# Performance work log

Hardware: AMD Instinct MI355X
Metric: run time of the kernel (lower is better)

The kernel has to match this reference:

```python
import jax, jax.numpy as jnp
import numpy as np

MUL = 32          # channel multiplicity
N_NODES = 50000
N_EDGES = 800000
IN_DIM = 4 * MUL      # 32x0e + 32x1o (ir_mul layout: 1o block is (3, MUL))
SH_DIM = 4            # 0e + 1o
W_DIM = 5 * MUL       # 5 CG paths, per-channel weights
OUT_DIM = 7 * MUL     # 32x0e + 32x1o + 32x1e
INV_SQRT3 = 0.5773502691896258
INV_SQRT2 = 0.7071067811865476


def setup_inputs() -> dict:
    key = jax.random.key(0)
    k1, k2, k3, k4 = jax.random.split(key, 4)
    node_features = jax.random.normal(k1, (N_NODES, IN_DIM), dtype=jnp.float32)
    edge_angular = jax.random.normal(k2, (N_EDGES, SH_DIM), dtype=jnp.float32)
    edge_index = jax.random.randint(k3, (N_EDGES, 2), 0, N_NODES, dtype=jnp.int64)
    tp_weights = jax.random.normal(k4, (N_EDGES, W_DIM), dtype=jnp.float32)
    return {"node_features": node_features, "edge_angular": edge_angular,
            "edge_index": edge_index, "tp_weights": tp_weights}


def reference(node_features, edge_angular, edge_index, tp_weights):
    n_nodes = node_features.shape[0]
    src = edge_index[:, 0]
    dst = edge_index[:, 1]

    # gather sender node features per edge
    h = node_features[src]                       # (E, 4*MUL)
    h0 = h[:, :MUL]                              # (E, MUL)       32x0e
    h1 = h[:, MUL:].reshape(-1, 3, MUL)          # (E, 3, MUL)    32x1o, ir_mul layout

    y0 = edge_angular[:, 0:1]                    # (E, 1)   0e
    y1 = edge_angular[:, 1:4]                    # (E, 3)   1o

    w = tp_weights.reshape(-1, 5, MUL)           # (E, 5, MUL) per-path per-channel

    # path 0: 0e (x) 0e -> 0e ; path 3: 1o (x) 1o -> 0e (dot / sqrt(3))
    dot = jnp.einsum('emc,em->ec', h1, y1)       # (E, MUL)
    out0e = w[:, 0] * h0 * y0 + w[:, 3] * (INV_SQRT3 * dot)

    # path 1: 0e (x) 1o -> 1o ; path 2: 1o (x) 0e -> 1o
    out1o = (w[:, 1][:, None, :] * h0[:, None, :] * y1[:, :, None]
             + w[:, 2][:, None, :] * h1 * y0[:, :, None])     # (E, 3, MUL)

    # path 4: 1o (x) 1o -> 1e (cross / sqrt(2))
    c0 = h1[:, 1] * y1[:, 2, None] - h1[:, 2] * y1[:, 1, None]
    c1 = h1[:, 2] * y1[:, 0, None] - h1[:, 0] * y1[:, 2, None]
    c2 = h1[:, 0] * y1[:, 1, None] - h1[:, 1] * y1[:, 0, None]
    cross = jnp.stack([c0, c1, c2], axis=1)                   # (E, 3, MUL)
    out1e = w[:, 4][:, None, :] * (INV_SQRT2 * cross)

    msg = jnp.concatenate([out0e,
                           out1o.reshape(-1, 3 * MUL),
                           out1e.reshape(-1, 3 * MUL)], axis=1)  # (E, 7*MUL)

    # scatter-add messages into receiver nodes (size_out = n_nodes)
    out = jax.ops.segment_sum(msg, dst, num_segments=n_nodes)    # (N, 7*MUL)
    return out
```

## Files before the change

kernel.cpp:

```cpp
#include <hip/hip_runtime.h>


#define IN_DIM 128
#define W_DIM 160
#define OUT_DIM 224

__device__ __forceinline__ float elem(const float4& v, int i) {
    return ((const float*)&v)[i];
}

__global__ void __launch_bounds__(256) hist_dst(
    const int* __restrict__ eidx, int* __restrict__ counts, int n_edges)
{
    int e = blockIdx.x * blockDim.x + threadIdx.x;
    if (e >= n_edges) return;
    atomicAdd(counts + eidx[2 * e + 1], 1);
}

__global__ void __launch_bounds__(1024) scan_counts(
    int* __restrict__ counts,
    int* __restrict__ cursor,
    int n)
{
    __shared__ int buf[1024];
    __shared__ int carry_s;
    int tid = threadIdx.x;
    if (tid == 0) carry_s = 0;
    __syncthreads();

    for (int base = 0; base < n; base += 1024) {
        int idx = base + tid;
        int x = (idx < n) ? counts[idx] : 0;
        buf[tid] = x;
        __syncthreads();
        #pragma unroll
        for (int off = 1; off < 1024; off <<= 1) {
            int v = (tid >= off) ? buf[tid - off] : 0;
            __syncthreads();
            buf[tid] += v;
            __syncthreads();
        }
        int carry = carry_s;
        int excl = buf[tid] - x + carry;
        if (idx < n) {
            counts[idx] = excl;
            cursor[idx] = excl;
        }
        int chunk_total = buf[1023];
        __syncthreads();
        if (tid == 0) carry_s = carry + chunk_total;
        __syncthreads();
    }
    if (tid == 0) counts[n] = carry_s;
}

__global__ void __launch_bounds__(256) scatter_edges(
    const int* __restrict__ eidx, int* __restrict__ cursor,
    int2* __restrict__ pairs, int n_edges)
{
    int e = blockIdx.x * blockDim.x + threadIdx.x;
    if (e >= n_edges) return;
    int src = eidx[2 * e];
    int dst = eidx[2 * e + 1];
    int pos = atomicAdd(cursor + dst, 1);
    pairs[pos] = make_int2(e, src);
}

__global__ void __launch_bounds__(256) gather_nodes(
    const float* __restrict__ nf,
    const float* __restrict__ ang,
    const float* __restrict__ w,
    const int*  __restrict__ offsets,
    const int2* __restrict__ pairs,
    float* __restrict__ out,
    int n_nodes)
{
    const float INV_SQRT3 = 0.5773502691896258f;
    const float INV_SQRT2 = 0.7071067811865476f;

    int gtid = blockIdx.x * blockDim.x + threadIdx.x;
    int node = gtid >> 6;
    if (node >= n_nodes) return;
    int lane = threadIdx.x & 63;
    int c    = lane & 31;
    int half = lane >> 5;

    int start = offsets[node];
    int end   = offsets[node + 1];

    float a0 = 0.f, a1 = 0.f, a2 = 0.f, a3 = 0.f, a4 = 0.f, a5 = 0.f, a6 = 0.f;

    for (int i = start + half; i < end; i += 2) {
        int2 p = pairs[i];
        int e = p.x, s = p.y;

        float4 y = *(const float4*)(ang + 4 * (size_t)e);

        const float* hp = nf + (size_t)s * IN_DIM + c;
        float h0 = hp[0];
        float ha = hp[32];
        float hb = hp[64];
        float hc = hp[96];

        const float* wp = w + (size_t)e * W_DIM + c;
        float w0 = wp[0];
        float w1 = wp[32];
        float w2 = wp[64];
        float w3 = wp[96];
        float w4 = wp[128];

        float dot = ha * y.y + hb * y.z + hc * y.w;
        a0 += w0 * h0 * y.x + w3 * (INV_SQRT3 * dot);
        a1 += w1 * h0 * y.y + w2 * ha * y.x;
        a2 += w1 * h0 * y.z + w2 * hb * y.x;
        a3 += w1 * h0 * y.w + w2 * hc * y.x;
        float w4s = w4 * INV_SQRT2;
        a4 += w4s * (hb * y.w - hc * y.z);
        a5 += w4s * (hc * y.y - ha * y.w);
        a6 += w4s * (ha * y.z - hb * y.y);
    }

    a0 += __shfl_xor(a0, 32);
    a1 += __shfl_xor(a1, 32);
    a2 += __shfl_xor(a2, 32);
    a3 += __shfl_xor(a3, 32);
    a4 += __shfl_xor(a4, 32);
    a5 += __shfl_xor(a5, 32);
    a6 += __shfl_xor(a6, 32);

    if (half == 0) {
        float* op = out + (size_t)node * OUT_DIM + c;
        op[0]   = a0;
        op[32]  = a1;
        op[64]  = a2;
        op[96]  = a3;
        op[128] = a4;
        op[160] = a5;
        op[192] = a6;
    }
}

__global__ void __launch_bounds__(256) conv_tp_edges_atomic(
    const float* __restrict__ nf,
    const float* __restrict__ ang,
    const int*   __restrict__ eidx,
    const float* __restrict__ w,
    float* __restrict__ out,
    int n_edges)
{
    const float INV_SQRT3 = 0.5773502691896258f;
    const float INV_SQRT2 = 0.7071067811865476f;

    int tid = blockIdx.x * blockDim.x + threadIdx.x;
    int e = tid >> 3;
    int t = tid & 7;
    if (e >= n_edges) return;

    int src = eidx[2 * e];
    int dst = eidx[2 * e + 1];
    float4 y = *(const float4*)(ang + 4 * (size_t)e);

    const float* hp = nf + (size_t)src * IN_DIM + 4 * t;
    float4 h0  = *(const float4*)(hp);
    float4 h1a = *(const float4*)(hp + 32);
    float4 h1b = *(const float4*)(hp + 64);
    float4 h1c = *(const float4*)(hp + 96);

    const float* wp = w + (size_t)e * W_DIM + 4 * t;
    float4 w0 = *(const float4*)(wp);
    float4 w1 = *(const float4*)(wp + 32);
    float4 w2 = *(const float4*)(wp + 64);
    float4 w3 = *(const float4*)(wp + 96);
    float4 w4 = *(const float4*)(wp + 128);

    float* op = out + (size_t)dst * OUT_DIM + 4 * t;

    #pragma unroll
    for (int i = 0; i < 4; ++i) {
        float h0c = elem(h0, i), ha = elem(h1a, i), hb = elem(h1b, i), hc = elem(h1c, i);
        float dot = ha * y.y + hb * y.z + hc * y.w;
        atomicAdd(op + i, elem(w0, i) * h0c * y.x + elem(w3, i) * (INV_SQRT3 * dot));
        float w1c = elem(w1, i), w2c = elem(w2, i);
        atomicAdd(op + 32 + i, w1c * h0c * y.y + w2c * ha * y.x);
        atomicAdd(op + 64 + i, w1c * h0c * y.z + w2c * hb * y.x);
        atomicAdd(op + 96 + i, w1c * h0c * y.w + w2c * hc * y.x);
        float w4c = elem(w4, i) * INV_SQRT2;
        atomicAdd(op + 128 + i, w4c * (hb * y.w - hc * y.z));
        atomicAdd(op + 160 + i, w4c * (hc * y.y - ha * y.w));
        atomicAdd(op + 192 + i, w4c * (ha * y.z - hb * y.y));
    }
}

extern "C" void kernel_launch(void* const* d_in, const int* in_sizes, int n_in,
                              void* d_out, int out_size, void* d_ws, size_t ws_size,
                              hipStream_t stream) {
    const float* nf   = (const float*)d_in[0];
    const float* ang  = (const float*)d_in[1];
    const int*   eidx = (const int*)d_in[2];
    const float* w    = (const float*)d_in[3];
    float* out = (float*)d_out;

    int n_edges = in_sizes[2] / 2;
    int n_nodes = out_size / OUT_DIM;

    size_t off_counts = 0;
    size_t off_cursor = off_counts + (size_t)(n_nodes + 1);
    size_t off_pairs  = (off_cursor + (size_t)n_nodes + 1) & ~(size_t)1;
    size_t ints_needed = off_pairs + 2 * (size_t)n_edges;
    size_t bytes_needed = ints_needed * sizeof(int);

    if (ws_size < bytes_needed) {
        hipMemsetAsync(d_out, 0, (size_t)out_size * sizeof(float), stream);
        int threads_total = n_edges * 8;
        int grid = (threads_total + 255) / 256;
        conv_tp_edges_atomic<<<grid, 256, 0, stream>>>(nf, ang, eidx, w, out, n_edges);
        return;
    }

    int* counts  = (int*)d_ws + off_counts;
    int* cursor  = (int*)d_ws + off_cursor;
    int2* pairs  = (int2*)((int*)d_ws + off_pairs);

    hipMemsetAsync(counts, 0, (size_t)(n_nodes + 1) * sizeof(int), stream);

    int grid_e = (n_edges + 255) / 256;
    hist_dst<<<grid_e, 256, 0, stream>>>(eidx, counts, n_edges);
    scan_counts<<<1, 1024, 0, stream>>>(counts, cursor, n_nodes);
    scatter_edges<<<grid_e, 256, 0, stream>>>(eidx, cursor, pairs, n_edges);

    int threads_total = n_nodes * 64;
    int grid_g = (threads_total + 255) / 256;
    gather_nodes<<<grid_g, 256, 0, stream>>>(nf, ang, w, counts, pairs, out, n_nodes);
}
```

Baseline: 902.9 us.

## Parallelize CSR prefix scan and unroll gather loop with nontemporal accesses

Replaces the single-block serial-chunk scan over node counts with a three-stage multi-block scan (block sums, scan of block sums, final per-block scan) using wavefront shuffles. Edge index loads become int2 vector loads. The gather loop is unrolled to process two edges per iteration, and the streaming weights, angular data and output use nontemporal loads and stores. This aims to remove the serialized scan bottleneck and improve memory-level parallelism, at the cost of extra kernel launches and a workspace slot for block sums.

```diff
diff --git a/kernel.cpp b/kernel.cpp
--- a/kernel.cpp
+++ b/kernel.cpp
@@ -5,65 +5,102 @@
 #define W_DIM 160
 #define OUT_DIM 224
 
+typedef float vf4 __attribute__((ext_vector_type(4)));
+
 __device__ __forceinline__ float elem(const float4& v, int i) {
     return ((const float*)&v)[i];
 }
 
 __global__ void __launch_bounds__(256) hist_dst(
-    const int* __restrict__ eidx, int* __restrict__ counts, int n_edges)
+    const int2* __restrict__ eidx2, int* __restrict__ counts, int n_edges)
 {
     int e = blockIdx.x * blockDim.x + threadIdx.x;
     if (e >= n_edges) return;
-    atomicAdd(counts + eidx[2 * e + 1], 1);
-}
-
-__global__ void __launch_bounds__(1024) scan_counts(
-    int* __restrict__ counts,
-    int* __restrict__ cursor,
-    int n)
-{
-    __shared__ int buf[1024];
+    atomicAdd(counts + eidx2[e].y, 1);
+}
+
+__global__ void __launch_bounds__(256) block_sums(
+    const int* __restrict__ counts, int* __restrict__ bsums, int n)
+{
+    int idx = blockIdx.x * 256 + threadIdx.x;
+    int x = (idx < n) ? counts[idx] : 0;
+    #pragma unroll
+    for (int off = 1; off < 64; off <<= 1) x += __shfl_xor(x, off);
+    __shared__ int ws[4];
+    if ((threadIdx.x & 63) == 0) ws[threadIdx.x >> 6] = x;
+    __syncthreads();
+    if (threadIdx.x == 0) bsums[blockIdx.x] = ws[0] + ws[1] + ws[2] + ws[3];
+}
+
+__global__ void __launch_bounds__(256) scan_block_sums(
+    int* __restrict__ bsums, int* __restrict__ total_out, int nb)
+{
+    __shared__ int wsum[4];
     __shared__ int carry_s;
     int tid = threadIdx.x;
+    int lane = tid & 63, wid = tid >> 6;
     if (tid == 0) carry_s = 0;
     __syncthreads();
 
-    for (int base = 0; base < n; base += 1024) {
+    for (int base = 0; base < nb; base += 256) {
         int idx = base + tid;
-        int x = (idx < n) ? counts[idx] : 0;
-        buf[tid] = x;
+        int x = (idx < nb) ? bsums[idx] : 0;
+        int incl = x;
+        #pragma unroll
+        for (int off = 1; off < 64; off <<= 1) {
+            int v = __shfl_up(incl, off);
+            if (lane >= off) incl += v;
+        }
+        if (lane == 63) wsum[wid] = incl;
         __syncthreads();
+        int wpre = 0;
         #pragma unroll
-        for (int off = 1; off < 1024; off <<= 1) {
-            int v = (tid >= off) ? buf[tid - off] : 0;
-            __syncthreads();
-            buf[tid] += v;
-            __syncthreads();
-        }
+        for (int k = 0; k < 4; ++k) if (k < wid) wpre += wsum[k];
         int carry = carry_s;
-        int excl = buf[tid] - x + carry;
-        if (idx < n) {
-            counts[idx] = excl;
-            cursor[idx] = excl;
-        }
-        int chunk_total = buf[1023];
+        int excl = incl - x + wpre + carry;
+        if (idx < nb) bsums[idx] = excl;
         __syncthreads();
-        if (tid == 0) carry_s = carry + chunk_total;
+        if (tid == 255) carry_s = carry + wpre + incl;
         __syncthreads();
     }
-    if (tid == 0) counts[n] = carry_s;
+    if (tid == 0) *total_out = carry_s;
+}
+
+__global__ void __launch_bounds__(256) scan_final(
+    int* __restrict__ counts, int* __restrict__ cursor,
+    const int* __restrict__ bsums, int n)
+{
+    int idx = blockIdx.x * 256 + threadIdx.x;
+    int x = (idx < n) ? counts[idx] : 0;
+    int lane = threadIdx.x & 63, wid = threadIdx.x >> 6;
+    int incl = x;
+    #pragma unroll
+    for (int off = 1; off < 64; off <<= 1) {
+        int v = __shfl_up(incl, off);
+        if (lane >= off) incl += v;
+    }
+    __shared__ int wsum[4];
+    if (lane == 63) wsum[wid] = incl;
+    __syncthreads();
+    int wpre = 0;
+    #pragma unroll
+    for (int k = 0; k < 4; ++k) if (k < wid) wpre += wsum[k];
+    int excl = incl - x + wpre + bsums[blockIdx.x];
+    if (idx < n) {
+        counts[idx] = excl;
+        cursor[idx] = excl;
+    }
 }
 
 __global__ void __launch_bounds__(256) scatter_edges(
-    const int* __restrict__ eidx, int* __restrict__ cursor,
+    const int2* __restrict__ eidx2, int* __restrict__ cursor,
     int2* __restrict__ pairs, int n_edges)
 {
     int e = blockIdx.x * blockDim.x + threadIdx.x;
     if (e >= n_edges) return;
-    int src = eidx[2 * e];
-    int dst = eidx[2 * e + 1];
-    int pos = atomicAdd(cursor + dst, 1);
-    pairs[pos] = make_int2(e, src);
+    int2 sd = eidx2[e];
+    int pos = atomicAdd(cursor + sd.y, 1);
+    pairs[pos] = make_int2(e, sd.x);
 }
 
 __global__ void __launch_bounds__(256) gather_nodes(
@@ -90,35 +127,40 @@
 
     float a0 = 0.f, a1 = 0.f, a2 = 0.f, a3 = 0.f, a4 = 0.f, a5 = 0.f, a6 = 0.f;
 
-    for (int i = start + half; i < end; i += 2) {
-        int2 p = pairs[i];
+    auto body = [&](int2 p) {
         int e = p.x, s = p.y;
-
-        float4 y = *(const float4*)(ang + 4 * (size_t)e);
-
+        vf4 y = __builtin_nontemporal_load((const vf4*)(ang + 4 * (size_t)e));
         const float* hp = nf + (size_t)s * IN_DIM + c;
         float h0 = hp[0];
         float ha = hp[32];
         float hb = hp[64];
         float hc = hp[96];
-
         const float* wp = w + (size_t)e * W_DIM + c;
-        float w0 = wp[0];
-        float w1 = wp[32];
-        float w2 = wp[64];
-        float w3 = wp[96];
-        float w4 = wp[128];
-
-        float dot = ha * y.y + hb * y.z + hc * y.w;
-        a0 += w0 * h0 * y.x + w3 * (INV_SQRT3 * dot);
-        a1 += w1 * h0 * y.y + w2 * ha * y.x;
-        a2 += w1 * h0 * y.z + w2 * hb * y.x;
-        a3 += w1 * h0 * y.w + w2 * hc * y.x;
+        float w0 = __builtin_nontemporal_load(wp);
+        float w1 = __builtin_nontemporal_load(wp + 32);
+        float w2 = __builtin_nontemporal_load(wp + 64);
+        float w3 = __builtin_nontemporal_load(wp + 96);
+        float w4 = __builtin_nontemporal_load(wp + 128);
+
+        float dot = ha * y[1] + hb * y[2] + hc * y[3];
+        a0 += w0 * h0 * y[0] + w3 * (INV_SQRT3 * dot);
+        a1 += w1 * h0 * y[1] + w2 * ha * y[0];
+        a2 += w1 * h0 * y[2] + w2 * hb * y[0];
+        a3 += w1 * h0 * y[3] + w2 * hc * y[0];
         float w4s = w4 * INV_SQRT2;
-        a4 += w4s * (hb * y.w - hc * y.z);
-        a5 += w4s * (hc * y.y - ha * y.w);
-        a6 += w4s * (ha * y.z - hb * y.y);
-    }
+        a4 += w4s * (hb * y[3] - hc * y[2]);
+        a5 += w4s * (hc * y[1] - ha * y[3]);
+        a6 += w4s * (ha * y[2] - hb * y[1]);
+    };
+
+    int i = start + half;
+    for (; i + 2 < end; i += 4) {
+        int2 pa = pairs[i];
+        int2 pb = pairs[i + 2];
+        body(pa);
+        body(pb);
+    }
+    if (i < end) body(pairs[i]);
 
     a0 += __shfl_xor(a0, 32);
     a1 += __shfl_xor(a1, 32);
@@ -130,13 +172,13 @@
 
     if (half == 0) {
         float* op = out + (size_t)node * OUT_DIM + c;
-        op[0]   = a0;
-        op[32]  = a1;
-        op[64]  = a2;
-        op[96]  = a3;
-        op[128] = a4;
-        op[160] = a5;
-        op[192] = a6;
+        __builtin_nontemporal_store(a0, op);
+        __builtin_nontemporal_store(a1, op + 32);
+        __builtin_nontemporal_store(a2, op + 64);
+        __builtin_nontemporal_store(a3, op + 96);
+        __builtin_nontemporal_store(a4, op + 128);
+        __builtin_nontemporal_store(a5, op + 160);
+        __builtin_nontemporal_store(a6, op + 192);
     }
 }
 
@@ -202,10 +244,12 @@
 
     int n_edges = in_sizes[2] / 2;
     int n_nodes = out_size / OUT_DIM;
+    int nb = (n_nodes + 255) / 256;
 
     size_t off_counts = 0;
     size_t off_cursor = off_counts + (size_t)(n_nodes + 1);
-    size_t off_pairs  = (off_cursor + (size_t)n_nodes + 1) & ~(size_t)1;
+    size_t off_bsums  = off_cursor + (size_t)n_nodes;
+    size_t off_pairs  = (off_bsums + (size_t)nb + 1) & ~(size_t)1;
     size_t ints_needed = off_pairs + 2 * (size_t)n_edges;
     size_t bytes_needed = ints_needed * sizeof(int);
 
@@ -219,14 +263,17 @@
 
     int* counts  = (int*)d_ws + off_counts;
     int* cursor  = (int*)d_ws + off_cursor;
+    int* bsums   = (int*)d_ws + off_bsums;
     int2* pairs  = (int2*)((int*)d_ws + off_pairs);
 
     hipMemsetAsync(counts, 0, (size_t)(n_nodes + 1) * sizeof(int), stream);
 
     int grid_e = (n_edges + 255) / 256;
-    hist_dst<<<grid_e, 256, 0, stream>>>(eidx, counts, n_edges);
-    scan_counts<<<1, 1024, 0, stream>>>(counts, cursor, n_nodes);
-    scatter_edges<<<grid_e, 256, 0, stream>>>(eidx, cursor, pairs, n_edges);
+    hist_dst<<<grid_e, 256, 0, stream>>>((const int2*)eidx, counts, n_edges);
+    block_sums<<<nb, 256, 0, stream>>>(counts, bsums, n_nodes);
+    scan_block_sums<<<1, 256, 0, stream>>>(bsums, counts + n_nodes, nb);
+    scan_final<<<nb, 256, 0, stream>>>(counts, cursor, bsums, n_nodes);
+    scatter_edges<<<grid_e, 256, 0, stream>>>((const int2*)eidx, cursor, pairs, n_edges);
 
     int threads_total = n_nodes * 64;
     int grid_g = (threads_total + 255) / 256;
```

Result: faster. 806.8 us (-10.6%).
